# Performance work log

Measured on AMD Instinct MI355X. Metric: run time of the kernel, lower is better.

## Reference

```python
import jax, jax.numpy as jnp
import numpy as np

B, D, L, H, T = 256, 512, 8, 8, 71
DH = D // H
SCALE = 0.01

def _lrelu(x):
    return jax.nn.leaky_relu(x, 0.2)

def _rms(x, dims, w):
    return w * x * jax.lax.rsqrt(jnp.mean(x * x, axis=dims, keepdims=True) + 1e-6)

def _conv(x, w, b, pad):
    y = jax.lax.conv_general_dilated(x, w, (1, 1), pad, dimension_numbers=('NCHW', 'OIHW', 'NCHW'))
    return y + b[None, :, None, None]

def _mha(x, qkv, nw):
    b_, d_, t_ = x.shape
    # einsum 'bdt,nhdD->nbhtD' -> (3,B,H,T,dh)
    y = jnp.einsum('bdt,nhdD->nbhtD', _lrelu(x), qkv)
    y = _rms(y, -2, nw)  # RMSNorm over the token axis (torch dim=-2)
    q, k, v = y[0], y[1], y[2]
    attn = jax.nn.softmax(jnp.einsum('bhtd,bhTd->bhtT', q, k) / np.float32(np.sqrt(DH)), axis=-1)
    out = jnp.einsum('bhtT,bhTd->bhdt', attn, v)  # (B,H,dh,T)
    return out.reshape(b_, d_, t_)

def _convblock(x, w1, b1, w2, b2, nw):
    b_, d_, t_ = x.shape
    y = x.reshape(b_, d_, 8, 8)
    y = _conv(_lrelu(y), w1, b1, 'SAME')
    y = _rms(y, (-1, -2), nw)
    y = _conv(_lrelu(y), w2, b2, 'SAME')
    return y.reshape(b_, d_, t_)

def _forward(fen, move, rank_emb, file_emb, fen_emb, move_emb, abs_emb, ln_w, ln_b, emb_qkv, emb_norm_w, qkv, mha_norm_w, conv1_w, conv1_b, conv2_w, conv2_b, cb_norm_w, out_norm_w, co1_w, co1_b, co2_w, co2_b):
    pos = (rank_emb + file_emb).reshape(64, D)
    mv = (pos[move] + move_emb) * 0.58          # (B,2,D)
    f = fen_emb[fen]                             # (B,133,D)
    board = 0.5 * (f[:, :64] + f[:, 64:128] + pos)
    x = jnp.concatenate([board, f[:, 128:], mv], axis=1) + abs_emb  # (B,71,D)
    x = jnp.swapaxes(x, -1, -2)                  # (B,D,71)
    mu = jnp.mean(x, -1, keepdims=True)
    var = jnp.mean((x - mu) ** 2, -1, keepdims=True)
    x = (x - mu) * jax.lax.rsqrt(var + 1e-5) * ln_w + ln_b  # LayerNorm over T=71
    y = _mha(x, emb_qkv, emb_norm_w)
    x = x[:, :, :64] + y[:, :, :64]              # keep the 64 board squares
    for i in range(L):
        x = x + _convblock(x, conv1_w[i], conv1_b[i], conv2_w[i], conv2_b[i], cb_norm_w[i])
        x = x + _mha(x, qkv[i], mha_norm_w[i])
    x = x.reshape(B, D, 8, 8)
    x = _conv(_lrelu(x), co1_w, co1_b, 'SAME')
    x = _rms(x, (-1, -2), out_norm_w)
    x = _conv(_lrelu(x), co2_w, co2_b, 'VALID')  # (B,1,1,1)
    return x.reshape(-1)

def setup_inputs():
    key = jax.random.key(0)
    ks = jax.random.split(key, 16)
    n = lambda k, s, sc: jax.random.normal(k, s, dtype=jnp.float32) * sc
    return {
        'fen': jax.random.randint(ks[0], (B, 133), 0, 17),
        'move': jax.random.randint(ks[1], (B, 2), 0, 64),
        'rank_emb': n(ks[2], (8, 1, D), SCALE),
        'file_emb': n(ks[3], (1, 8, D), SCALE),
        'fen_emb': n(ks[4], (17, D), SCALE),
        'move_emb': n(ks[5], (2, D), SCALE),
        'abs_emb': n(ks[6], (71, D), SCALE),
        'ln_w': jnp.ones((71,), jnp.float32),
        'ln_b': jnp.zeros((71,), jnp.float32),
        'emb_qkv': n(ks[7], (3, H, D, DH), SCALE),
        'emb_norm_w': jnp.ones((1,), jnp.float32),
        'qkv': n(ks[8], (L, 3, H, D, DH), SCALE * 0.64),
        'mha_norm_w': jnp.ones((L, 1), jnp.float32),
        'conv1_w': n(ks[9], (L, D, D, 3, 3), SCALE * 0.64),
        'conv1_b': jnp.zeros((L, D), jnp.float32),
        'conv2_w': n(ks[10], (L, D, D, 3, 3), SCALE * 0.64),
        'conv2_b': jnp.zeros((L, D), jnp.float32),
        'cb_norm_w': jnp.ones((L, 1), jnp.float32),
        'out_norm_w': jnp.ones((1,), jnp.float32),
        'co1_w': n(ks[11], (2 * D, D, 3, 3), SCALE),
        'co1_b': jnp.zeros((2 * D,), jnp.float32),
        'co2_w': n(ks[12], (1, 2 * D, 8, 8), SCALE),
        'co2_b': jnp.zeros((1,), jnp.float32),
    }

def reference(fen, move, rank_emb, file_emb, fen_emb, move_emb, abs_emb, ln_w, ln_b, emb_qkv, emb_norm_w, qkv, mha_norm_w, conv1_w, conv1_b, conv2_w, conv2_b, cb_norm_w, out_norm_w, co1_w, co1_b, co2_w, co2_b):
    return _forward(fen, move, rank_emb, file_emb, fen_emb, move_emb, abs_emb, ln_w, ln_b, emb_qkv, emb_norm_w, qkv, mha_norm_w, conv1_w, conv1_b, conv2_w, conv2_b, cb_norm_w, out_norm_w, co1_w, co1_b, co2_w, co2_b)
```

## Files before the change

kernel.cpp:

```cpp
#include <hip/hip_runtime.h>
#include <hip/hip_bf16.h>
#include <cstdint>
#include <cstddef>


typedef float f32x4 __attribute__((ext_vector_type(4)));
typedef short short8 __attribute__((ext_vector_type(8)));

__device__ __forceinline__ float lrelu(float v) { return v > 0.f ? v : 0.2f * v; }
__device__ __forceinline__ __hip_bfloat16 tobf(float v) { return __float2bfloat16(v); }
__device__ __forceinline__ float frombf(__hip_bfloat16 v) { return __bfloat162float(v); }

__global__ __launch_bounds__(256) void repack_qkv_w(
    const float* __restrict__ emb_qkv, const float* __restrict__ qkvw,
    __hip_bfloat16* __restrict__ Wq)
{
  int o = blockIdx.x * 256 + threadIdx.x;
  int L = o / (1536 * 512);
  int rem = o - L * 1536 * 512;
  int j = rem >> 9;
  int d = rem & 511;
  int n = j >> 9, h = (j >> 6) & 7, dh = j & 63;
  float v;
  if (L == 0) v = emb_qkv[(((n * 8 + h) * 512 + d) << 6) + dh];
  else        v = qkvw[((((size_t)(L - 1) * 3 + n) * 8 + h) * 512 + d) * 64 + dh];
  Wq[o] = tobf(v);
}

__global__ __launch_bounds__(256) void repack_conv_w2(
    const float* __restrict__ w, __hip_bfloat16* __restrict__ W2, int COUT)
{
  const int t = blockIdx.x * 256 + threadIdx.x;
  if (t >= (COUT << 6)) return;
  const int lr = t & 15;
  const int cbg = (t >> 4) & 63;
  const int oj = t >> 10;
  const int cc = cbg >> 3, ks = (cbg >> 2) & 1, lg = cbg & 3;
  const int o = oj * 16 + lr;
  const int NJ = COUT >> 4;
  const float* src = w + ((size_t)o * 512 + cbg * 8) * 9;
  #pragma unroll
  for (int k = 0; k < 9; ++k) {
    __hip_bfloat16 tmp[8];
    #pragma unroll
    for (int e = 0; e < 8; ++e) tmp[e] = tobf(src[e * 9 + k]);
    size_t di = ((((size_t)cc * 9 + k) * NJ + oj) * 2 + ks) * 512 + (lg * 16 + lr) * 8;
    *(uint4*)&W2[di] = *(const uint4*)tmp;
  }
}

__global__ __launch_bounds__(256) void build_ln_kernel(
    const int* __restrict__ fen, const int* __restrict__ move,
    const float* __restrict__ rank_emb, const float* __restrict__ file_emb,
    const float* __restrict__ fen_emb, const float* __restrict__ move_emb,
    const float* __restrict__ abs_emb, const float* __restrict__ lnw,
    const float* __restrict__ lnb, __hip_bfloat16* __restrict__ X71)
{
  const int gid = blockIdx.x * 256 + threadIdx.x;
  const int b = gid >> 9, d = gid & 511;
  const int* fb = fen + b * 133;

  float sum = 0.f, sq = 0.f, mu = 0.f, rstd = 0.f;
  #pragma unroll 1
  for (int pass = 0; pass < 2; ++pass) {
    if (pass) {
      mu = sum * (1.f / 71.f);
      float var = sq * (1.f / 71.f) - mu * mu;
      rstd = rsqrtf(var + 1e-5f);
    }
    #pragma unroll 1
    for (int t = 0; t < 71; ++t) {
      float a = abs_emb[t * 512 + d];
      float v;
      if (t < 64) {
        float pos = rank_emb[(t >> 3) * 512 + d] + file_emb[(t & 7) * 512 + d];
        v = 0.5f * (fen_emb[fb[t] * 512 + d] + fen_emb[fb[64 + t] * 512 + d] + pos) + a;
      } else if (t < 69) {
        v = fen_emb[fb[t + 64] * 512 + d] + a;
      } else {
        int j = t - 69;
        int s = move[b * 2 + j];
        float pos = rank_emb[(s >> 3) * 512 + d] + file_emb[(s & 7) * 512 + d];
        v = (pos + move_emb[j * 512 + d]) * 0.58f + a;
      }
      if (pass) X71[(size_t)gid * 71 + t] = tobf((v - mu) * rstd * lnw[t] + lnb[t]);
      else { sum += v; sq += v * v; }
    }
  }
}

template <int T, int TP, bool INBF>
__global__ __launch_bounds__(256) void proj_kernel(
    const void* __restrict__ xin, const __hip_bfloat16* __restrict__ Wq,
    const float* __restrict__ nw,
    __hip_bfloat16* __restrict__ qk, __hip_bfloat16* __restrict__ vT)
{
  const int b  = blockIdx.x / 6;
  const int jb = (blockIdx.x % 6) * 256;
  const int tid = threadIdx.x;
  const int lane = tid & 63, wv = tid >> 6;
  const int lr = lane & 15, lg = lane >> 4;

  __shared__ __hip_bfloat16 xt[TP * 72];
  __shared__ __hip_bfloat16 wl[256 * 72];

  constexpr int MI = TP / 16;
  f32x4 acc[MI][4];
  #pragma unroll
  for (int mi = 0; mi < MI; ++mi)
    #pragma unroll
    for (int ni = 0; ni < 4; ++ni) acc[mi][ni] = {0.f, 0.f, 0.f, 0.f};

  for (int c0 = 0; c0 < 512; c0 += 64) {
    if constexpr (INBF) {
      const __hip_bfloat16* x = (const __hip_bfloat16*)xin;
      for (int i = tid; i < 64 * TP; i += 256) {
        int d = i / TP, t = i - d * TP;
        float v = (t < T) ? lrelu(frombf(x[((size_t)(b * 512 + c0 + d)) * T + t])) : 0.f;
        xt[t * 72 + d] = tobf(v);
      }
    } else {
      const float* x = (const float*)xin;
      for (int i = tid; i < 64 * TP; i += 256) {
        int d = i >> 6, t = i & 63;
        float v = lrelu(x[((size_t)(b * 512 + c0 + d)) * 64 + t]);
        xt[t * 72 + d] = tobf(v);
      }
    }
    for (int i = tid; i < 2048; i += 256) {
      int j = i >> 3, cb = i & 7;
      *(uint4*)&wl[j * 72 + cb * 8] =
          *(const uint4*)&Wq[(size_t)(jb + j) * 512 + c0 + cb * 8];
    }
    __syncthreads();
    #pragma unroll
    for (int ks = 0; ks < 2; ++ks) {
      short8 a[MI], bb[4];
      #pragma unroll
      for (int mi = 0; mi < MI; ++mi)
        a[mi] = *(const short8*)&xt[(mi * 16 + lr) * 72 + ks * 32 + lg * 8];
      #pragma unroll
      for (int ni = 0; ni < 4; ++ni)
        bb[ni] = *(const short8*)&wl[(wv * 64 + ni * 16 + lr) * 72 + ks * 32 + lg * 8];
      #pragma unroll
      for (int mi = 0; mi < MI; ++mi)
        #pragma unroll
        for (int ni = 0; ni < 4; ++ni)
          acc[mi][ni] = __builtin_amdgcn_mfma_f32_16x16x32_bf16(
              a[mi], bb[ni], acc[mi][ni], 0, 0, 0);
    }
    __syncthreads();
  }

  #pragma unroll
  for (int ni = 0; ni < 4; ++ni) {
    const int j = jb + wv * 64 + ni * 16 + lr;
    float ss = 0.f;
    #pragma unroll
    for (int mi = 0; mi < MI; ++mi)
      #pragma unroll
      for (int r = 0; r < 4; ++r) ss += acc[mi][ni][r] * acc[mi][ni][r];
    ss += __shfl_xor(ss, 16);
    ss += __shfl_xor(ss, 32);
    const float sc = nw[0] * rsqrtf(ss * (1.f / T) + 1e-6f);
    if (j < 1024) {
      #pragma unroll
      for (int mi = 0; mi < MI; ++mi)
        #pragma unroll
        for (int r = 0; r < 4; ++r) {
          int t = mi * 16 + lg * 4 + r;
          if (TP == T || t < T)
            qk[((size_t)b * T + t) * 1024 + j] = tobf(acc[mi][ni][r] * sc);
        }
    } else {
      const int jj = j - 1024;
      #pragma unroll
      for (int mi = 0; mi < MI; ++mi)
        #pragma unroll
        for (int r = 0; r < 4; ++r) {
          int t = mi * 16 + lg * 4 + r;
          vT[((size_t)b * 512 + jj) * TP + t] = tobf(acc[mi][ni][r] * sc);
        }
    }
  }
}

template <int T, bool RESBF>
__global__ __launch_bounds__(256) void attn2_kernel(
    const __hip_bfloat16* __restrict__ qk,
    const __hip_bfloat16* __restrict__ vT,
    const void* __restrict__ res, float* __restrict__ out)
{
  constexpr int TP = (T == 71) ? 80 : 64;
  constexpr int TK = (T + 31) / 32;
  constexpr int RS = 72;
  constexpr int PS = TK * 32 + 8;
  constexpr int KR = (T == 71) ? 80 : 64;
  constexpr int SC = (T == 71) ? 82 : 66;
  constexpr int NCF = KR / 16;
  constexpr int NFW = (NCF + 3) / 4;
  constexpr int RANGE = (TK * 32) / 4;

  constexpr int Q_OFF = 0;
  constexpr int K_OFF = Q_OFF + 64 * RS * 2;
  constexpr int V_OFF = K_OFF + KR * RS * 2;
  constexpr int S_OFF = V_OFF + 64 * PS * 2;
  constexpr int BYTES = S_OFF + 64 * SC * 4;
  __shared__ __align__(16) char smem[BYTES];
  __hip_bfloat16* qs = (__hip_bfloat16*)(smem + Q_OFF);
  __hip_bfloat16* ksh = (__hip_bfloat16*)(smem + K_OFF);
  __hip_bfloat16* vs = (__hip_bfloat16*)(smem + V_OFF);
  float* ss = (float*)(smem + S_OFF);
  __hip_bfloat16* ps = (__hip_bfloat16*)(smem + S_OFF);

  const int b = blockIdx.x >> 3, h = blockIdx.x & 7;
  const int tid = threadIdx.x;
  const int lane = tid & 63, wv = tid >> 6;
  const int lr = lane & 15, lg = lane >> 4;

  for (int i = tid; i < BYTES / 16; i += 256) ((uint4*)smem)[i] = uint4{0, 0, 0, 0};
  __syncthreads();

  const __hip_bfloat16* qb = qk + (size_t)b * T * 1024 + h * 64;
  for (int v = tid; v < 512; v += 256) {
    int t = v >> 3, d0 = (v & 7) * 8;
    *(uint4*)&qs[t * RS + d0] = *(const uint4*)&qb[(size_t)t * 1024 + d0];
  }
  for (int v = tid; v < T * 8; v += 256) {
    int t = v >> 3, d0 = (v & 7) * 8;
    *(uint4*)&ksh[t * RS + d0] = *(const uint4*)&qb[(size_t)t * 1024 + 512 + d0];
  }
  constexpr int VV = TP / 8;
  for (int v = tid; v < 64 * VV; v += 256) {
    int dh = v / VV, tc = (v - dh * VV) * 8;
    *(uint4*)&vs[dh * PS + tc] =
        *(const uint4*)&vT[((size_t)b * 512 + h * 64 + dh) * TP + tc];
  }
  __syncthreads();

  f32x4 sacc[NFW][4];
  #pragma unroll
  for (int fi = 0; fi < NFW; ++fi)
    #pragma unroll
    for (int mi = 0; mi < 4; ++mi) sacc[fi][mi] = {0.f, 0.f, 0.f, 0.f};
  #pragma unroll
  for (int ks2 = 0; ks2 < 2; ++ks2) {
    short8 a[4];
    #pragma unroll
    for (int mi = 0; mi < 4; ++mi)
      a[mi] = *(const short8*)&qs[(mi * 16 + lr) * RS + ks2 * 32 + lg * 8];
    #pragma unroll
    for (int fi = 0; fi < NFW; ++fi) {
      const int f = wv + fi * 4;
      if (f < NCF) {
        short8 bb = *(const short8*)&ksh[(f * 16 + lr) * RS + ks2 * 32 + lg * 8];
        #pragma unroll
        for (int mi = 0; mi < 4; ++mi)
          sacc[fi][mi] = __builtin_amdgcn_mfma_f32_16x16x32_bf16(
              a[mi], bb, sacc[fi][mi], 0, 0, 0);
      }
    }
  }
  #pragma unroll
  for (int fi = 0; fi < NFW; ++fi) {
    const int f = wv + fi * 4;
    if (f < NCF) {
      #pragma unroll
      for (int mi = 0; mi < 4; ++mi)
        #pragma unroll
        for (int r = 0; r < 4; ++r)
          ss[(mi * 16 + lg * 4 + r) * SC + f * 16 + lr] = sacc[fi][mi][r] * 0.125f;
    }
  }
  __syncthreads();

  {
    const int row = tid >> 2, q4 = tid & 3;
    float sv[RANGE];
    float mx = -3.0e38f;
    #pragma unroll
    for (int i = 0; i < RANGE; ++i) {
      int c = q4 * RANGE + i;
      sv[i] = (c < T) ? ss[row * SC + c] : -3.0e38f;
      mx = fmaxf(mx, sv[i]);
    }
    mx = fmaxf(mx, __shfl_xor(mx, 1));
    mx = fmaxf(mx, __shfl_xor(mx, 2));
    float sm = 0.f;
    #pragma unroll
    for (int i = 0; i < RANGE; ++i) {
      int c = q4 * RANGE + i;
      sv[i] = (c < T) ? __expf(sv[i] - mx) : 0.f;
      sm += sv[i];
    }
    sm += __shfl_xor(sm, 1);
    sm += __shfl_xor(sm, 2);
    const float inv = 1.f / sm;
    __syncthreads();
    #pragma unroll
    for (int i = 0; i < RANGE; ++i)
      ps[row * PS + q4 * RANGE + i] = tobf(sv[i] * inv);
  }
  __syncthreads();

  f32x4 oacc[4];
  #pragma unroll
  for (int mi = 0; mi < 4; ++mi) oacc[mi] = {0.f, 0.f, 0.f, 0.f};
  #pragma unroll
  for (int ks2 = 0; ks2 < TK; ++ks2) {
    short8 bb = *(const short8*)&vs[(wv * 16 + lr) * PS + ks2 * 32 + lg * 8];
    #pragma unroll
    for (int mi = 0; mi < 4; ++mi) {
      short8 a = *(const short8*)&ps[(mi * 16 + lr) * PS + ks2 * 32 + lg * 8];
      oacc[mi] = __builtin_amdgcn_mfma_f32_16x16x32_bf16(a, bb, oacc[mi], 0, 0, 0);
    }
  }

  const int dh = wv * 16 + lr;
  const size_t chb = (size_t)b * 512 + h * 64 + dh;
  #pragma unroll
  for (int mi = 0; mi < 4; ++mi) {
    const int t0 = mi * 16 + lg * 4;
    const size_t idx = chb * 64 + t0;
    f32x4 v = oacc[mi];
    if constexpr (RESBF) {
      const __hip_bfloat16* rb = (const __hip_bfloat16*)res + chb * T + t0;
      #pragma unroll
      for (int r = 0; r < 4; ++r) v[r] += frombf(rb[r]);
    } else {
      v += *(const f32x4*)&((const float*)res)[idx];
    }
    *(f32x4*)&out[idx] = v;
  }
}

template <bool RMSOUT, bool RESADD>
__global__ __launch_bounds__(256) void conv_mfma2(
    const float* __restrict__ x,
    const __hip_bfloat16* __restrict__ W2,
    const float* __restrict__ bias,
    const float* __restrict__ nw,
    const float* __restrict__ res,
    float* __restrict__ out,
    int COUT)
{
  const int ntc = COUT >> 8;
  const int b = blockIdx.x / ntc;
  const int nt = blockIdx.x - b * ntc;
  const int o0 = nt << 8;
  const int NJ = COUT >> 4;
  const int tid = threadIdx.x;
  const int lane = tid & 63, wv = tid >> 6;
  const int lr = lane & 15, lg = lane >> 4;

  __shared__ __hip_bfloat16 xt[2][100 * 72];

  f32x4 acc[4][4];
  #pragma unroll
  for (int mi = 0; mi < 4; ++mi)
    #pragma unroll
    for (int ni = 0; ni < 4; ++ni) acc[mi][ni] = {0.f, 0.f, 0.f, 0.f};

  for (int i = tid; i < 7200; i += 256) { xt[0][i] = tobf(0.f); xt[1][i] = tobf(0.f); }

  f32x4 sreg[4];
  const int s_ci = tid >> 4;
  const int s_p4 = (tid & 15) << 2;
  const int s_row = (((s_p4 >> 3) + 1) * 10 + (s_p4 & 7) + 1) * 72;

  #define STAGE_LOAD(cc_)                                                     \
    {                                                                         \
      const float* xb_ = x + ((size_t)b * 512 + (cc_) * 64 + s_ci) * 64 + s_p4; \
      _Pragma("unroll")                                                       \
      for (int u = 0; u < 4; ++u) sreg[u] = *(const f32x4*)&xb_[u * 1024];    \
    }
  #define STAGE_WRITE(buf_)                                                   \
    {                                                                         \
      _Pragma("unroll")                                                       \
      for (int u = 0; u < 4; ++u) {                                           \
        _Pragma("unroll")                                                     \
        for (int j = 0; j < 4; ++j)                                           \
          xt[buf_][s_row + j * 72 + s_ci + u * 16] = tobf(lrelu(sreg[u][j])); \
      }                                                                       \
    }

  STAGE_LOAD(0);
  __syncthreads();
  STAGE_WRITE(0);
  __syncthreads();

  const int ojb2 = ((o0 >> 4) + wv * 4) * 2;

  for (int cc = 0; cc < 8; ++cc) {
    const int cur = cc & 1;
    if (cc < 7) STAGE_LOAD(cc + 1);
    const __hip_bfloat16* xb = xt[cur];

    #pragma unroll
    for (int k = 0; k < 9; ++k) {
      const int dy = k / 3 - 1, dx = k - (k / 3) * 3 - 1;
      const int ii0 = (lr >> 3) + dy + 1;
      const int jj0 = (lr & 7) + dx + 1;
      const size_t slab = ((size_t)(cc * 9 + k) * NJ) * 2 + ojb2;
      short8 bv[2][4], av[2][4];
      #pragma unroll
      for (int ni = 0; ni < 4; ++ni)
        #pragma unroll
        for (int ks = 0; ks < 2; ++ks)
          bv[ks][ni] = *(const short8*)&W2[(slab + ni * 2 + ks) * 512 + lane * 8];
      #pragma unroll
      for (int ks = 0; ks < 2; ++ks)
        #pragma unroll
        for (int mi = 0; mi < 4; ++mi)
          av[ks][mi] = *(const short8*)&xb[((ii0 + mi * 2) * 10 + jj0) * 72 + ks * 32 + lg * 8];
      #pragma unroll
      for (int ks = 0; ks < 2; ++ks)
        #pragma unroll
        for (int mi = 0; mi < 4; ++mi)
          #pragma unroll
          for (int ni = 0; ni < 4; ++ni)
            acc[mi][ni] = __builtin_amdgcn_mfma_f32_16x16x32_bf16(
                av[ks][mi], bv[ks][ni], acc[mi][ni], 0, 0, 0);
    }
    if (cc < 7) STAGE_WRITE(cur ^ 1);
    __syncthreads();
  }
  #undef STAGE_LOAD
  #undef STAGE_WRITE

  #pragma unroll
  for (int ni = 0; ni < 4; ++ni) {
    const int o = o0 + wv * 64 + ni * 16 + lr;
    const float bvs = bias[o];
    float sc = 1.f;
    if constexpr (RMSOUT) {
      float ssq = 0.f;
      #pragma unroll
      for (int mi = 0; mi < 4; ++mi)
        #pragma unroll
        for (int r = 0; r < 4; ++r) {
          float v = acc[mi][ni][r] + bvs;
          ssq += v * v;
        }
      ssq += __shfl_xor(ssq, 16);
      ssq += __shfl_xor(ssq, 32);
      sc = nw[0] * rsqrtf(ssq * (1.f / 64.f) + 1e-6f);
    }
    #pragma unroll
    for (int mi = 0; mi < 4; ++mi) {
      size_t idx = ((size_t)b * COUT + o) * 64 + mi * 16 + lg * 4;
      f32x4 v;
      #pragma unroll
      for (int r = 0; r < 4; ++r) v[r] = (acc[mi][ni][r] + bvs) * sc;
      if constexpr (RESADD) v += *(const f32x4*)&res[idx];
      *(f32x4*)&out[idx] = v;
    }
  }
}

__global__ __launch_bounds__(256) void co2_kernel(
    const float* __restrict__ xf, const float* __restrict__ w,
    const float* __restrict__ cb, float* __restrict__ out)
{
  const int b = blockIdx.x, tid = threadIdx.x;
  const float* xb = xf + (size_t)b * 65536;
  float acc = 0.f;
  for (int i = tid; i < 65536; i += 256)
    acc += lrelu(xb[i]) * w[i];
  #pragma unroll
  for (int off = 32; off; off >>= 1) acc += __shfl_down(acc, off);
  __shared__ float red[4];
  if ((tid & 63) == 0) red[tid >> 6] = acc;
  __syncthreads();
  if (tid == 0) out[b] = red[0] + red[1] + red[2] + red[3] + cb[0];
}

extern "C" void kernel_launch(void* const* d_in, const int* in_sizes, int n_in,
                              void* d_out, int out_size, void* d_ws, size_t ws_size,
                              hipStream_t stream)
{
  const int*   fen        = (const int*)d_in[0];
  const int*   move       = (const int*)d_in[1];
  const float* rank_emb   = (const float*)d_in[2];
  const float* file_emb   = (const float*)d_in[3];
  const float* fen_emb    = (const float*)d_in[4];
  const float* move_emb   = (const float*)d_in[5];
  const float* abs_emb    = (const float*)d_in[6];
  const float* ln_w       = (const float*)d_in[7];
  const float* ln_b       = (const float*)d_in[8];
  const float* emb_qkv    = (const float*)d_in[9];
  const float* emb_norm_w = (const float*)d_in[10];
  const float* qkvw_in    = (const float*)d_in[11];
  const float* mha_norm_w = (const float*)d_in[12];
  const float* conv1_w    = (const float*)d_in[13];
  const float* conv1_b    = (const float*)d_in[14];
  const float* conv2_w    = (const float*)d_in[15];
  const float* conv2_b    = (const float*)d_in[16];
  const float* cb_norm_w  = (const float*)d_in[17];
  const float* out_norm_w = (const float*)d_in[18];
  const float* co1_w      = (const float*)d_in[19];
  const float* co1_b      = (const float*)d_in[20];
  const float* co2_w      = (const float*)d_in[21];
  const float* co2_b      = (const float*)d_in[22];
  float* out = (float*)d_out;

  char* base = (char*)d_ws;
  __hip_bfloat16* X71 = (__hip_bfloat16*)base;
  float* X64 = (float*)(base + 18612224);
  float* T1  = (float*)(base + 18612224 + 33554432);
  __hip_bfloat16* Wq = (__hip_bfloat16*)(base + 18612224 + 33554432 + 67108864);
  __hip_bfloat16* qk2 = (__hip_bfloat16*)T1;
  __hip_bfloat16* vTb = (__hip_bfloat16*)((char*)T1 + 37224448);
  float* F1 = T1;
  __hip_bfloat16* WcA = (__hip_bfloat16*)base;
  __hip_bfloat16* WcB = (__hip_bfloat16*)(base + 4718592);

  repack_qkv_w<<<27648, 256, 0, stream>>>(emb_qkv, qkvw_in, Wq);

  build_ln_kernel<<<512, 256, 0, stream>>>(fen, move, rank_emb, file_emb,
                                           fen_emb, move_emb, abs_emb,
                                           ln_w, ln_b, X71);
  proj_kernel<71, 80, true><<<1536, 256, 0, stream>>>(X71, Wq, emb_norm_w, qk2, vTb);
  attn2_kernel<71, true><<<2048, 256, 0, stream>>>(qk2, vTb, X71, X64);

  for (int l = 0; l < 8; ++l) {
    repack_conv_w2<<<128, 256, 0, stream>>>(conv1_w + (size_t)l * 512 * 512 * 9,
                                            WcA, 512);
    conv_mfma2<true, false><<<512, 256, 0, stream>>>(X64, WcA, conv1_b + l * 512,
                                                     cb_norm_w + l, nullptr, T1, 512);
    repack_conv_w2<<<128, 256, 0, stream>>>(conv2_w + (size_t)l * 512 * 512 * 9,
                                            WcB, 512);
    conv_mfma2<false, true><<<512, 256, 0, stream>>>(T1, WcB, conv2_b + l * 512,
                                                     nullptr, X64, X64, 512);
    proj_kernel<64, 64, false><<<1536, 256, 0, stream>>>(
        X64, Wq + (size_t)(l + 1) * 1536 * 512, mha_norm_w + l, qk2, vTb);
    attn2_kernel<64, false><<<2048, 256, 0, stream>>>(qk2, vTb, X64, X64);
  }

  repack_conv_w2<<<256, 256, 0, stream>>>(co1_w, WcA, 1024);
  conv_mfma2<true, false><<<1024, 256, 0, stream>>>(X64, WcA, co1_b,
                                                    out_norm_w, nullptr, F1, 1024);
  co2_kernel<<<256, 256, 0, stream>>>(F1, co2_w, co2_b, out);
}
```

Measured before the change: 2.891 ms.

## Pre-swizzle QKV weights into MFMA fragment layout and double-buffer proj64 activations

Splits the QKV weight repack in two. The per-layer weights are now stored in an MFMA-fragment order, so the new proj64 kernel can load B operands straight from global memory into registers instead of staging them in shared memory. The activation tile is double-buffered in LDS, with register prefetch of the next chunk overlapping the current MFMAs. This removes weight LDS traffic and one barrier per chunk, but relies on global-memory or cache latency for the weight loads.

```diff
diff --git a/kernel.cpp b/kernel.cpp
--- a/kernel.cpp
+++ b/kernel.cpp
@@ -11,20 +11,33 @@
 __device__ __forceinline__ __hip_bfloat16 tobf(float v) { return __float2bfloat16(v); }
 __device__ __forceinline__ float frombf(__hip_bfloat16 v) { return __bfloat162float(v); }
 
-__global__ __launch_bounds__(256) void repack_qkv_w(
-    const float* __restrict__ emb_qkv, const float* __restrict__ qkvw,
-    __hip_bfloat16* __restrict__ Wq)
+__global__ __launch_bounds__(256) void repack_qkv_w0(
+    const float* __restrict__ emb_qkv, __hip_bfloat16* __restrict__ Wq0)
 {
   int o = blockIdx.x * 256 + threadIdx.x;
-  int L = o / (1536 * 512);
-  int rem = o - L * 1536 * 512;
-  int j = rem >> 9;
-  int d = rem & 511;
+  int j = o >> 9, d = o & 511;
   int n = j >> 9, h = (j >> 6) & 7, dh = j & 63;
-  float v;
-  if (L == 0) v = emb_qkv[(((n * 8 + h) * 512 + d) << 6) + dh];
-  else        v = qkvw[((((size_t)(L - 1) * 3 + n) * 8 + h) * 512 + d) * 64 + dh];
-  Wq[o] = tobf(v);
+  Wq0[o] = tobf(emb_qkv[(((n * 8 + h) * 512 + d) << 6) + dh]);
+}
+
+__global__ __launch_bounds__(256) void repack_qkv_w2(
+    const float* __restrict__ qkvw, __hip_bfloat16* __restrict__ Wq2)
+{
+  const int t = blockIdx.x * 256 + threadIdx.x;
+  const int lane = t & 63;
+  const int nj = (t >> 6) % 96;
+  int rest = (t >> 6) / 96;
+  const int ks = rest & 1;
+  const int kc = (rest >> 1) & 7;
+  const int L = rest >> 4;
+  const int j = nj * 16 + (lane & 15);
+  const int d0 = kc * 64 + ks * 32 + (lane >> 4) * 8;
+  const int n = j >> 9, h = (j >> 6) & 7, dh = j & 63;
+  const float* src = qkvw + ((((size_t)L * 3 + n) * 8 + h) * 512 + d0) * 64 + dh;
+  __hip_bfloat16 tmp[8];
+  #pragma unroll
+  for (int e = 0; e < 8; ++e) tmp[e] = tobf(src[(size_t)e * 64]);
+  *(uint4*)&Wq2[(size_t)t * 8] = *(const uint4*)tmp;
 }
 
 __global__ __launch_bounds__(256) void repack_conv_w2(
@@ -89,9 +102,9 @@
   }
 }
 
-template <int T, int TP, bool INBF>
-__global__ __launch_bounds__(256) void proj_kernel(
-    const void* __restrict__ xin, const __hip_bfloat16* __restrict__ Wq,
+template <int T, int TP>
+__global__ __launch_bounds__(256) void proj71_kernel(
+    const __hip_bfloat16* __restrict__ xin, const __hip_bfloat16* __restrict__ Wq,
     const float* __restrict__ nw,
     __hip_bfloat16* __restrict__ qk, __hip_bfloat16* __restrict__ vT)
 {
@@ -112,20 +125,10 @@
     for (int ni = 0; ni < 4; ++ni) acc[mi][ni] = {0.f, 0.f, 0.f, 0.f};
 
   for (int c0 = 0; c0 < 512; c0 += 64) {
-    if constexpr (INBF) {
-      const __hip_bfloat16* x = (const __hip_bfloat16*)xin;
-      for (int i = tid; i < 64 * TP; i += 256) {
-        int d = i / TP, t = i - d * TP;
-        float v = (t < T) ? lrelu(frombf(x[((size_t)(b * 512 + c0 + d)) * T + t])) : 0.f;
-        xt[t * 72 + d] = tobf(v);
-      }
-    } else {
-      const float* x = (const float*)xin;
-      for (int i = tid; i < 64 * TP; i += 256) {
-        int d = i >> 6, t = i & 63;
-        float v = lrelu(x[((size_t)(b * 512 + c0 + d)) * 64 + t]);
-        xt[t * 72 + d] = tobf(v);
-      }
+    for (int i = tid; i < 64 * TP; i += 256) {
+      int d = i / TP, t = i - d * TP;
+      float v = (t < T) ? lrelu(frombf(xin[((size_t)(b * 512 + c0 + d)) * T + t])) : 0.f;
+      xt[t * 72 + d] = tobf(v);
     }
     for (int i = tid; i < 2048; i += 256) {
       int j = i >> 3, cb = i & 7;
@@ -169,7 +172,7 @@
         #pragma unroll
         for (int r = 0; r < 4; ++r) {
           int t = mi * 16 + lg * 4 + r;
-          if (TP == T || t < T)
+          if (t < T)
             qk[((size_t)b * T + t) * 1024 + j] = tobf(acc[mi][ni][r] * sc);
         }
     } else {
@@ -180,6 +183,111 @@
         for (int r = 0; r < 4; ++r) {
           int t = mi * 16 + lg * 4 + r;
           vT[((size_t)b * 512 + jj) * TP + t] = tobf(acc[mi][ni][r] * sc);
+        }
+    }
+  }
+}
+
+__global__ __launch_bounds__(256) void proj64_kernel(
+    const float* __restrict__ x,
+    const __hip_bfloat16* __restrict__ Wq2,
+    const float* __restrict__ nw,
+    __hip_bfloat16* __restrict__ qk, __hip_bfloat16* __restrict__ vT)
+{
+  const int b    = blockIdx.x / 6;
+  const int jseg = blockIdx.x % 6;
+  const int tid = threadIdx.x;
+  const int lane = tid & 63, wv = tid >> 6;
+  const int lr = lane & 15, lg = lane >> 4;
+
+  __shared__ __hip_bfloat16 xt[2][64 * 72];
+
+  f32x4 acc[4][4];
+  #pragma unroll
+  for (int mi = 0; mi < 4; ++mi)
+    #pragma unroll
+    for (int ni = 0; ni < 4; ++ni) acc[mi][ni] = {0.f, 0.f, 0.f, 0.f};
+
+  f32x4 sreg[4];
+  const int s_d  = tid >> 4;
+  const int s_t4 = (tid & 15) << 2;
+
+  #define PSTAGE_LOAD(kc_)                                                    \
+    {                                                                         \
+      const float* xb_ = x + ((size_t)b * 512 + (kc_) * 64 + s_d) * 64 + s_t4; \
+      _Pragma("unroll")                                                       \
+      for (int u = 0; u < 4; ++u) sreg[u] = *(const f32x4*)&xb_[u * 1024];    \
+    }
+  #define PSTAGE_WRITE(buf_)                                                  \
+    {                                                                         \
+      _Pragma("unroll")                                                       \
+      for (int u = 0; u < 4; ++u) {                                           \
+        _Pragma("unroll")                                                     \
+        for (int j = 0; j < 4; ++j)                                           \
+          xt[buf_][(s_t4 + j) * 72 + s_d + u * 16] = tobf(lrelu(sreg[u][j])); \
+      }                                                                       \
+    }
+
+  PSTAGE_LOAD(0);
+  PSTAGE_WRITE(0);
+  __syncthreads();
+
+  const int njb0 = jseg * 16 + wv * 4;
+
+  for (int kc = 0; kc < 8; ++kc) {
+    const int cur = kc & 1;
+    if (kc < 7) PSTAGE_LOAD(kc + 1);
+    const __hip_bfloat16* xb = xt[cur];
+    #pragma unroll
+    for (int ks = 0; ks < 2; ++ks) {
+      short8 bv[4], av[4];
+      #pragma unroll
+      for (int ni = 0; ni < 4; ++ni)
+        bv[ni] = *(const short8*)
+            &Wq2[((((size_t)kc * 2 + ks) * 96) + njb0 + ni) * 512 + lane * 8];
+      #pragma unroll
+      for (int mi = 0; mi < 4; ++mi)
+        av[mi] = *(const short8*)&xb[(mi * 16 + lr) * 72 + ks * 32 + lg * 8];
+      #pragma unroll
+      for (int mi = 0; mi < 4; ++mi)
+        #pragma unroll
+        for (int ni = 0; ni < 4; ++ni)
+          acc[mi][ni] = __builtin_amdgcn_mfma_f32_16x16x32_bf16(
+              av[mi], bv[ni], acc[mi][ni], 0, 0, 0);
+    }
+    if (kc < 7) PSTAGE_WRITE(cur ^ 1);
+    __syncthreads();
+  }
+  #undef PSTAGE_LOAD
+  #undef PSTAGE_WRITE
+
+  #pragma unroll
+  for (int ni = 0; ni < 4; ++ni) {
+    const int j = jseg * 256 + wv * 64 + ni * 16 + lr;
+    float ss = 0.f;
+    #pragma unroll
+    for (int mi = 0; mi < 4; ++mi)
+      #pragma unroll
+      for (int r = 0; r < 4; ++r) ss += acc[mi][ni][r] * acc[mi][ni][r];
+    ss += __shfl_xor(ss, 16);
+    ss += __shfl_xor(ss, 32);
+    const float sc = nw[0] * rsqrtf(ss * (1.f / 64.f) + 1e-6f);
+    if (j < 1024) {
+      #pragma unroll
+      for (int mi = 0; mi < 4; ++mi)
+        #pragma unroll
+        for (int r = 0; r < 4; ++r) {
+          int t = mi * 16 + lg * 4 + r;
+          qk[((size_t)b * 64 + t) * 1024 + j] = tobf(acc[mi][ni][r] * sc);
+        }
+    } else {
+      const int jj = j - 1024;
+      #pragma unroll
+      for (int mi = 0; mi < 4; ++mi)
+        #pragma unroll
+        for (int r = 0; r < 4; ++r) {
+          int t = mi * 16 + lg * 4 + r;
+          vT[((size_t)b * 512 + jj) * 64 + t] = tobf(acc[mi][ni][r] * sc);
         }
     }
   }
@@ -508,19 +616,21 @@
   __hip_bfloat16* X71 = (__hip_bfloat16*)base;
   float* X64 = (float*)(base + 18612224);
   float* T1  = (float*)(base + 18612224 + 33554432);
-  __hip_bfloat16* Wq = (__hip_bfloat16*)(base + 18612224 + 33554432 + 67108864);
+  __hip_bfloat16* Wq0 = (__hip_bfloat16*)(base + 119275520);
+  __hip_bfloat16* Wq2 = (__hip_bfloat16*)(base + 120848384);
   __hip_bfloat16* qk2 = (__hip_bfloat16*)T1;
   __hip_bfloat16* vTb = (__hip_bfloat16*)((char*)T1 + 37224448);
   float* F1 = T1;
   __hip_bfloat16* WcA = (__hip_bfloat16*)base;
   __hip_bfloat16* WcB = (__hip_bfloat16*)(base + 4718592);
 
-  repack_qkv_w<<<27648, 256, 0, stream>>>(emb_qkv, qkvw_in, Wq);
+  repack_qkv_w0<<<3072, 256, 0, stream>>>(emb_qkv, Wq0);
+  repack_qkv_w2<<<3072, 256, 0, stream>>>(qkvw_in, Wq2);
 
   build_ln_kernel<<<512, 256, 0, stream>>>(fen, move, rank_emb, file_emb,
                                            fen_emb, move_emb, abs_emb,
                                            ln_w, ln_b, X71);
-  proj_kernel<71, 80, true><<<1536, 256, 0, stream>>>(X71, Wq, emb_norm_w, qk2, vTb);
+  proj71_kernel<71, 80><<<1536, 256, 0, stream>>>(X71, Wq0, emb_norm_w, qk2, vTb);
   attn2_kernel<71, true><<<2048, 256, 0, stream>>>(qk2, vTb, X71, X64);
 
   for (int l = 0; l < 8; ++l) {
@@ -532,8 +642,8 @@
                                             WcB, 512);
     conv_mfma2<false, true><<<512, 256, 0, stream>>>(T1, WcB, conv2_b + l * 512,
                                                      nullptr, X64, X64, 512);
-    proj_kernel<64, 64, false><<<1536, 256, 0, stream>>>(
-        X64, Wq + (size_t)(l + 1) * 1536 * 512, mha_norm_w + l, qk2, vTb);
+    proj64_kernel<<<1536, 256, 0, stream>>>(X64, Wq2 + (size_t)l * 786432,
+                                            mha_norm_w + l, qk2, vTb);
     attn2_kernel<64, false><<<2048, 256, 0, stream>>>(qk2, vTb, X64, X64);
   }
 
```

Result: faster. 2.690 ms (median of 2 runs) (-6.9%).
